# Optimization experiments

Hardware: AMD Instinct MI355X
Metric: run time of the kernel (lower is better)

The kernel has to match this reference:

```python
import jax, jax.numpy as jnp
import numpy as np

B, S, D, H = 2, 4096, 512, 8
HD = D // H


def setup_inputs() -> dict:
    key = jax.random.key(0)
    ks = jax.random.split(key, 11)
    s = 1.0 / np.sqrt(D)
    return {
        "queries": jax.random.normal(ks[0], (B, S, D), jnp.float32),
        "keys": jax.random.normal(ks[1], (B, S, D), jnp.float32),
        "values": jax.random.normal(ks[2], (B, S, D), jnp.float32),
        "Wq": jax.random.normal(ks[3], (D, D), jnp.float32) * s,
        "bq": jnp.zeros((D,), jnp.float32),
        "Wk": jax.random.normal(ks[4], (D, D), jnp.float32) * s,
        "bk": jnp.zeros((D,), jnp.float32),
        "Wv": jax.random.normal(ks[5], (D, D), jnp.float32) * s,
        "bv": jnp.zeros((D,), jnp.float32),
        "Wo": jax.random.normal(ks[6], (D, D), jnp.float32) * s,
        "bo": jnp.zeros((D,), jnp.float32),
    }


def reference(queries, keys, values, Wq, bq, Wk, bk, Wv, bv, Wo, bo):
    b = queries.shape[0]
    # Linear projections (torch Linear: x @ W.T + b; here W stored as [in, out])
    q = (queries @ Wq + bq).reshape(b, -1, H, HD)   # [B, Sq, H, HD]
    k = (keys @ Wk + bk).reshape(b, -1, H, HD)       # [B, Sk, H, HD]
    v = (values @ Wv + bv).reshape(b, -1, H, HD)     # [B, Sk, H, HD]
    logits = jnp.einsum('bqhd,bkhd->bhqk', q, k) / jnp.sqrt(jnp.float32(HD))
    attn = jax.nn.softmax(logits, axis=-1)           # [B, H, Sq, Sk]  (dropout_rate=0 -> identity)
    ctx = jnp.einsum('bhqk,bkhd->bqhd', attn, v).reshape(b, -1, H * HD)
    return ctx @ Wo + bo
```

## Files before the change

### kernel.cpp

```cpp
#include <hip/hip_runtime.h>
#include <hip/hip_bf16.h>

constexpr int B_  = 2;
constexpr int S_  = 4096;
constexpr int D_  = 512;
constexpr int H_  = 8;
constexpr int HD_ = 64;
constexpr int M_  = B_ * S_;

typedef __attribute__((ext_vector_type(8))) short short8;
typedef __attribute__((ext_vector_type(4))) float floatx4;

static __device__ __forceinline__ unsigned short f2bf(float f) {
    union { float f; unsigned u; } v; v.f = f;
    unsigned r = v.u + 0x7fffu + ((v.u >> 16) & 1u);
    return (unsigned short)(r >> 16);
}

static __device__ __forceinline__ unsigned pk2bf(float a, float b) {
#if __has_builtin(__builtin_amdgcn_cvt_pk_bf16_f32)
    typedef __attribute__((ext_vector_type(2))) __bf16 bf16x2_t;
    union { bf16x2_t v; unsigned u; } u;
    u.v = __builtin_amdgcn_cvt_pk_bf16_f32(a, b);
    return u.u;
#else
    return (unsigned)f2bf(a) | ((unsigned)f2bf(b) << 16);
#endif
}

#if __has_builtin(__builtin_amdgcn_exp2f)
#define EXP2(x) __builtin_amdgcn_exp2f(x)
#else
#define EXP2(x) exp2f(x)
#endif

#define QSCALE 0.18033688011110204f

__global__ __launch_bounds__(256) void wtrans_kernel(
    const float* __restrict__ Wq, const float* __restrict__ Wk,
    const float* __restrict__ Wv, const float* __restrict__ Wo,
    unsigned short* __restrict__ Tq, unsigned short* __restrict__ Tk,
    unsigned short* __restrict__ Tv, unsigned short* __restrict__ To) {
    const int z = blockIdx.z;
    const float* W = z == 0 ? Wq : (z == 1 ? Wk : (z == 2 ? Wv : Wo));
    unsigned short* Wt = z == 0 ? Tq : (z == 1 ? Tk : (z == 2 ? Tv : To));
    __shared__ float T[64][65];
    const int t = threadIdx.x;
    const int k0 = blockIdx.x * 64, n0 = blockIdx.y * 64;
#pragma unroll
    for (int i = 0; i < 4; ++i) {
        const int flat = t + 256 * i;
        const int kr = flat >> 4, nc = (flat & 15) * 4;
        float4 v = *(const float4*)&W[(size_t)(k0 + kr) * 512 + n0 + nc];
        T[kr][nc] = v.x; T[kr][nc + 1] = v.y; T[kr][nc + 2] = v.z; T[kr][nc + 3] = v.w;
    }
    __syncthreads();
#pragma unroll
    for (int i = 0; i < 4; ++i) {
        const int flat = t + 256 * i;
        const int nr = flat >> 4, kc = (flat & 15) * 4;
        ushort4 o4;
        o4.x = f2bf(T[kc][nr]);     o4.y = f2bf(T[kc + 1][nr]);
        o4.z = f2bf(T[kc + 2][nr]); o4.w = f2bf(T[kc + 3][nr]);
        *(ushort4*)&Wt[(size_t)(n0 + nr) * 512 + k0 + kc] = o4;
    }
}

__global__ __launch_bounds__(256, 2) void qkv_kernel(
    const float* __restrict__ Xq, const float* __restrict__ Xk, const float* __restrict__ Xv,
    const unsigned short* __restrict__ Tq, const unsigned short* __restrict__ Tk,
    const unsigned short* __restrict__ Tv,
    const float* __restrict__ bq, const float* __restrict__ bk, const float* __restrict__ bv,
    unsigned short* __restrict__ Oq, unsigned short* __restrict__ Ok,
    unsigned short* __restrict__ Ovt) {
    const int z = blockIdx.z;
    const float* A            = z == 0 ? Xq : (z == 1 ? Xk : Xv);
    const unsigned short* Wt  = z == 0 ? Tq : (z == 1 ? Tk : Tv);
    const float* bias         = z == 0 ? bq : (z == 1 ? bk : bv);
    unsigned short* out       = z == 0 ? Oq : (z == 1 ? Ok : Ovt);
    const float scale         = z == 0 ? QSCALE : 1.0f;

    const int tid = threadIdx.x;
    const int n0  = blockIdx.x * 128;
    const int m0  = blockIdx.y * 128;
    const int w   = tid >> 6;
    const int l   = tid & 63;
    const int wm  = (w >> 1) * 64;
    const int wn  = (w & 1) * 64;
    const int lm  = l & 15;
    const int lq  = l >> 4;

    const float* arow[4];
    const unsigned short* brow[4];
#pragma unroll
    for (int i = 0; i < 4; ++i) {
        arow[i] = &A[(size_t)(m0 + wm + i * 16 + lm) * 512 + lq * 8];
        brow[i] = &Wt[(size_t)(n0 + wn + i * 16 + lm) * 512 + lq * 8];
    }

    floatx4 acc[4][4];
#pragma unroll
    for (int i = 0; i < 4; ++i)
#pragma unroll
        for (int j = 0; j < 4; ++j) acc[i][j] = (floatx4)0.0f;

    float4 araw[4][2];
    short8 bnxt[4];
#pragma unroll
    for (int i = 0; i < 4; ++i) {
        araw[i][0] = *(const float4*)(arow[i]);
        araw[i][1] = *(const float4*)(arow[i] + 4);
        bnxt[i]    = *(const short8*)(brow[i]);
    }

    for (int kb = 0; kb < 16; ++kb) {
        short8 a_cur[4], b_cur[4];
#pragma unroll
        for (int i = 0; i < 4; ++i) {
            union { short8 s; unsigned u[4]; } pk;
            pk.u[0] = pk2bf(araw[i][0].x, araw[i][0].y);
            pk.u[1] = pk2bf(araw[i][0].z, araw[i][0].w);
            pk.u[2] = pk2bf(araw[i][1].x, araw[i][1].y);
            pk.u[3] = pk2bf(araw[i][1].z, araw[i][1].w);
            a_cur[i] = pk.s;
            b_cur[i] = bnxt[i];
        }
        if (kb < 15) {
            const int k1 = (kb + 1) * 32;
#pragma unroll
            for (int i = 0; i < 4; ++i) {
                araw[i][0] = *(const float4*)(arow[i] + k1);
                araw[i][1] = *(const float4*)(arow[i] + k1 + 4);
                bnxt[i]    = *(const short8*)(brow[i] + k1);
            }
        }
#pragma unroll
        for (int mi = 0; mi < 4; ++mi)
#pragma unroll
            for (int ni = 0; ni < 4; ++ni)
                acc[mi][ni] = __builtin_amdgcn_mfma_f32_16x16x32_bf16(
                    a_cur[mi], b_cur[ni], acc[mi][ni], 0, 0, 0);
    }

    float bias_n[4];
#pragma unroll
    for (int ni = 0; ni < 4; ++ni) bias_n[ni] = bias[n0 + wn + ni * 16 + lm];

#pragma unroll
    for (int mi = 0; mi < 4; ++mi) {
#pragma unroll
        for (int ni = 0; ni < 4; ++ni) {
            const int gn = n0 + wn + ni * 16 + lm;
            const int h = gn >> 6, hd = gn & 63;
            if (z == 2) {
                const int gm = m0 + wm + mi * 16 + lq * 4;
                const int b = gm >> 12, s = gm & 4095;
                ushort4 o4;
                o4.x = f2bf(acc[mi][ni][0] + bias_n[ni]);
                o4.y = f2bf(acc[mi][ni][1] + bias_n[ni]);
                o4.z = f2bf(acc[mi][ni][2] + bias_n[ni]);
                o4.w = f2bf(acc[mi][ni][3] + bias_n[ni]);
                *(ushort4*)&out[(((size_t)(b * 8 + h)) * 64 + hd) * 4096 + s] = o4;
            } else {
#pragma unroll
                for (int r = 0; r < 4; ++r) {
                    const int gm = m0 + wm + mi * 16 + lq * 4 + r;
                    const int b = gm >> 12, s = gm & 4095;
                    const float vv = (acc[mi][ni][r] + bias_n[ni]) * scale;
                    out[(((size_t)(b * 8 + h)) * 4096 + s) * 64 + hd] = f2bf(vv);
                }
            }
        }
    }
}

__global__ __launch_bounds__(512) void o_proj_kernel(
    const unsigned short* __restrict__ A, const unsigned short* __restrict__ Wt,
    const float* __restrict__ bias, float* __restrict__ outp) {
    const int tid = threadIdx.x;
    const int n0  = blockIdx.x * 128;
    const int m0  = blockIdx.y * 128;
    const int w   = tid >> 6;
    const int l   = tid & 63;
    const int wm  = (w >> 2) * 64;
    const int wn  = (w & 3) * 32;
    const int lm  = l & 15;
    const int lq  = l >> 4;

    const unsigned short* arow[4];
    const unsigned short* brow[2];
#pragma unroll
    for (int i = 0; i < 4; ++i)
        arow[i] = &A[(size_t)(m0 + wm + i * 16 + lm) * 512 + lq * 8];
#pragma unroll
    for (int i = 0; i < 2; ++i)
        brow[i] = &Wt[(size_t)(n0 + wn + i * 16 + lm) * 512 + lq * 8];

    floatx4 acc[4][2];
#pragma unroll
    for (int i = 0; i < 4; ++i)
#pragma unroll
        for (int j = 0; j < 2; ++j) acc[i][j] = (floatx4)0.0f;

    short8 anxt[4], bnxt[2];
#pragma unroll
    for (int i = 0; i < 4; ++i) anxt[i] = *(const short8*)(arow[i]);
#pragma unroll
    for (int i = 0; i < 2; ++i) bnxt[i] = *(const short8*)(brow[i]);

    for (int kb = 0; kb < 16; ++kb) {
        short8 a_cur[4], b_cur[2];
#pragma unroll
        for (int i = 0; i < 4; ++i) a_cur[i] = anxt[i];
#pragma unroll
        for (int i = 0; i < 2; ++i) b_cur[i] = bnxt[i];
        if (kb < 15) {
            const int k1 = (kb + 1) * 32;
#pragma unroll
            for (int i = 0; i < 4; ++i) anxt[i] = *(const short8*)(arow[i] + k1);
#pragma unroll
            for (int i = 0; i < 2; ++i) bnxt[i] = *(const short8*)(brow[i] + k1);
        }
#pragma unroll
        for (int mi = 0; mi < 4; ++mi)
#pragma unroll
            for (int ni = 0; ni < 2; ++ni)
                acc[mi][ni] = __builtin_amdgcn_mfma_f32_16x16x32_bf16(
                    a_cur[mi], b_cur[ni], acc[mi][ni], 0, 0, 0);
    }

    float bias_n[2];
#pragma unroll
    for (int ni = 0; ni < 2; ++ni) bias_n[ni] = bias[n0 + wn + ni * 16 + lm];

#pragma unroll
    for (int mi = 0; mi < 4; ++mi)
#pragma unroll
        for (int ni = 0; ni < 2; ++ni) {
            const int gn = n0 + wn + ni * 16 + lm;
#pragma unroll
            for (int r = 0; r < 4; ++r) {
                const int gm = m0 + wm + mi * 16 + lq * 4 + r;
                outp[(size_t)gm * 512 + gn] = acc[mi][ni][r] + bias_n[ni];
            }
        }
}

__global__ __launch_bounds__(256, 2) void flash_kernel(
    const unsigned short* __restrict__ Q, const unsigned short* __restrict__ K,
    const unsigned short* __restrict__ Vt, unsigned short* __restrict__ ctx) {
    __shared__ unsigned short Ks[64 * 64];
    __shared__ unsigned short Vs[64 * 64];
    __shared__ unsigned short Ps[4][16 * 64];

    const int tid = threadIdx.x;
    const int w   = tid >> 6;
    const int l   = tid & 63;
    const int lm  = l & 15;
    const int lq  = l >> 4;
    const int q0  = blockIdx.x * 128;
    const int bh  = blockIdx.y;

    const size_t base = (size_t)bh * S_ * HD_;
    const unsigned short* Qg = Q + base;
    const unsigned short* Kg = K + base;
    const unsigned short* Vg = Vt + base;

    short8 qf[2][2];
#pragma unroll
    for (int qn = 0; qn < 2; ++qn) {
        const unsigned short* qp = &Qg[(size_t)(q0 + w * 32 + qn * 16 + lm) * 64];
        qf[qn][0] = *(const short8*)(qp + lq * 8);
        qf[qn][1] = *(const short8*)(qp + 32 + lq * 8);
    }

    short8 ones;
#pragma unroll
    for (int j = 0; j < 8; ++j) ones[j] = (short)0x3F80;

    floatx4 o[2][4];
#pragma unroll
    for (int qn = 0; qn < 2; ++qn)
#pragma unroll
        for (int i = 0; i < 4; ++i) o[qn][i] = (floatx4)0.0f;
    floatx4 ls[2];
    ls[0] = (floatx4)0.0f; ls[1] = (floatx4)0.0f;

    const int sr  = tid >> 3, sch = tid & 7;
    const int sw0 = sr * 64 + ((sch ^ (sr & 7)) * 8);
    const int sw1 = (sr + 32) * 64 + ((sch ^ (sr & 7)) * 8);
    const int lm7 = lm & 7;

    short8 kr0, kr1, vr0, vr1;
    kr0 = *(const short8*)&Kg[(size_t)sr * 64 + sch * 8];
    kr1 = *(const short8*)&Kg[(size_t)(sr + 32) * 64 + sch * 8];
    vr0 = *(const short8*)&Vg[(size_t)sr * S_ + sch * 8];
    vr1 = *(const short8*)&Vg[(size_t)(sr + 32) * S_ + sch * 8];

    for (int kt = 0; kt < 64; ++kt) {
        __syncthreads();
        *(short8*)&Ks[sw0] = kr0;
        *(short8*)&Ks[sw1] = kr1;
        *(short8*)&Vs[sw0] = vr0;
        *(short8*)&Vs[sw1] = vr1;
        __syncthreads();
        if (kt < 63) {
            const int t1 = (kt + 1) * 64;
            kr0 = *(const short8*)&Kg[(size_t)(t1 + sr) * 64 + sch * 8];
            kr1 = *(const short8*)&Kg[(size_t)(t1 + sr + 32) * 64 + sch * 8];
            vr0 = *(const short8*)&Vg[(size_t)sr * S_ + t1 + sch * 8];
            vr1 = *(const short8*)&Vg[(size_t)(sr + 32) * S_ + t1 + sch * 8];
        }

        short8 kf[2][4];
#pragma unroll
        for (int ks = 0; ks < 2; ++ks)
#pragma unroll
            for (int ni = 0; ni < 4; ++ni)
                kf[ks][ni] = *(const short8*)&Ks[(ni * 16 + lm) * 64 +
                                                 (((ks * 4 + lq) ^ lm7) * 8)];

        floatx4 sf[2][4];
#pragma unroll
        for (int qn = 0; qn < 2; ++qn)
#pragma unroll
            for (int ni = 0; ni < 4; ++ni) sf[qn][ni] = (floatx4)0.0f;
#pragma unroll
        for (int ks = 0; ks < 2; ++ks)
#pragma unroll
            for (int qn = 0; qn < 2; ++qn)
#pragma unroll
                for (int ni = 0; ni < 4; ++ni)
                    sf[qn][ni] = __builtin_amdgcn_mfma_f32_16x16x32_bf16(
                        kf[ks][ni], qf[qn][ks], sf[qn][ni], 0, 0, 0);

        short8 vf[2][4];
#pragma unroll
        for (int c = 0; c < 2; ++c)
#pragma unroll
            for (int ni = 0; ni < 4; ++ni)
                vf[c][ni] = *(const short8*)&Vs[(ni * 16 + lm) * 64 +
                                                (((c * 4 + lq) ^ lm7) * 8)];

        unsigned short* Pw = &Ps[w][0];
#pragma unroll
        for (int qn = 0; qn < 2; ++qn) {
#pragma unroll
            for (int ni = 0; ni < 4; ++ni) {
                uint2 pv;
                pv.x = pk2bf(EXP2(sf[qn][ni][0]), EXP2(sf[qn][ni][1]));
                pv.y = pk2bf(EXP2(sf[qn][ni][2]), EXP2(sf[qn][ni][3]));
                *(uint2*)&Pw[lm * 64 + (((ni * 2 + (lq >> 1)) ^ lm7) * 8) + (lq & 1) * 4] = pv;
            }
#pragma unroll
            for (int c = 0; c < 2; ++c) {
                short8 pf = *(const short8*)&Pw[lm * 64 + (((c * 4 + lq) ^ lm7) * 8)];
                ls[qn] = __builtin_amdgcn_mfma_f32_16x16x32_bf16(ones, pf, ls[qn], 0, 0, 0);
#pragma unroll
                for (int ni = 0; ni < 4; ++ni)
                    o[qn][ni] = __builtin_amdgcn_mfma_f32_16x16x32_bf16(
                        vf[c][ni], pf, o[qn][ni], 0, 0, 0);
            }
        }
    }

    const int b = bh >> 3, h = bh & 7;
#pragma unroll
    for (int qn = 0; qn < 2; ++qn) {
        const float inv = 1.0f / ls[qn][0];
        const int q = q0 + w * 32 + qn * 16 + lm;
        const size_t rb = ((size_t)(b * S_ + q)) * 512 + h * 64;
#pragma unroll
        for (int ni = 0; ni < 4; ++ni) {
            union { ushort4 s; uint2 u; } o4;
            o4.u.x = pk2bf(o[qn][ni][0] * inv, o[qn][ni][1] * inv);
            o4.u.y = pk2bf(o[qn][ni][2] * inv, o[qn][ni][3] * inv);
            *(ushort4*)&ctx[rb + ni * 16 + lq * 4] = o4.s;
        }
    }
}

extern "C" void kernel_launch(void* const* d_in, const int* in_sizes, int n_in,
                              void* d_out, int out_size, void* d_ws, size_t ws_size,
                              hipStream_t stream) {
    const float* queries = (const float*)d_in[0];
    const float* keys    = (const float*)d_in[1];
    const float* values  = (const float*)d_in[2];
    const float* Wq = (const float*)d_in[3];
    const float* bq = (const float*)d_in[4];
    const float* Wk = (const float*)d_in[5];
    const float* bk = (const float*)d_in[6];
    const float* Wv = (const float*)d_in[7];
    const float* bv = (const float*)d_in[8];
    const float* Wo = (const float*)d_in[9];
    const float* bo = (const float*)d_in[10];

    unsigned short* wsq   = (unsigned short*)d_ws;
    unsigned short* wsk   = wsq   + (size_t)M_ * D_;
    unsigned short* wsvt  = wsk   + (size_t)M_ * D_;
    unsigned short* wsctx = wsvt  + (size_t)M_ * D_;
    unsigned short* wtq   = wsctx + (size_t)M_ * D_;
    unsigned short* wtk   = wtq   + (size_t)D_ * D_;
    unsigned short* wtv   = wtk   + (size_t)D_ * D_;
    unsigned short* wto   = wtv   + (size_t)D_ * D_;

    wtrans_kernel<<<dim3(8, 8, 4), dim3(256), 0, stream>>>(
        Wq, Wk, Wv, Wo, wtq, wtk, wtv, wto);

    qkv_kernel<<<dim3(D_ / 128, M_ / 128, 3), dim3(256), 0, stream>>>(
        queries, keys, values, wtq, wtk, wtv, bq, bk, bv, wsq, wsk, wsvt);

    flash_kernel<<<dim3(S_ / 128, B_ * H_), dim3(256), 0, stream>>>(wsq, wsk, wsvt, wsctx);

    o_proj_kernel<<<dim3(D_ / 128, M_ / 128), dim3(512), 0, stream>>>(
        wsctx, wto, bo, (float*)d_out);
}
```

Measured before the change: 291.3 us.

## Pre-cast inputs to bf16 and use LDS-staged swizzled GEMM for projections

Adds a separate kernel that casts the fp32 query/key/value inputs to bf16 once. The QKV and output projections now share one templated GEMM that stages 128x64 A and B tiles into shared memory with direct global-to-LDS loads and an XOR swizzle. Before, each wave read its operands straight from global memory and converted fp32 to bf16 inside the loop. Tiles are now shared across waves in a block, in exchange for an extra pass over the inputs and two syncthreads per k-step with no double buffering. Because the weight transposes are laid out contiguously, the QKV GEMM indexes Wq, Wk and Wv through a single pointer.

```diff
diff --git a/kernel.cpp b/kernel.cpp
--- a/kernel.cpp
+++ b/kernel.cpp
@@ -35,6 +35,31 @@
 #endif
 
 #define QSCALE 0.18033688011110204f
+
+static __device__ __forceinline__ void gl_lds16(const void* g, void* l) {
+    typedef __attribute__((address_space(1))) const unsigned GU;
+    typedef __attribute__((address_space(3))) unsigned LU;
+    __builtin_amdgcn_global_load_lds((GU*)g, (LU*)l, 16, 0, 0);
+}
+
+__global__ __launch_bounds__(256) void xcast_kernel(
+    const float* __restrict__ Xq, const float* __restrict__ Xk, const float* __restrict__ Xv,
+    unsigned short* __restrict__ Y) {
+    const int z = blockIdx.z;
+    const float* X = z == 0 ? Xq : (z == 1 ? Xk : Xv);
+    unsigned short* Yz = Y + (size_t)z * M_ * D_;
+    const int n8 = M_ * D_ / 8;
+    int i = blockIdx.x * 256 + threadIdx.x;
+    const int stride = gridDim.x * 256;
+    for (; i < n8; i += stride) {
+        float4 a = *(const float4*)&X[(size_t)i * 8];
+        float4 b = *(const float4*)&X[(size_t)i * 8 + 4];
+        union { short8 s; unsigned u[4]; } p;
+        p.u[0] = pk2bf(a.x, a.y); p.u[1] = pk2bf(a.z, a.w);
+        p.u[2] = pk2bf(b.x, b.y); p.u[3] = pk2bf(b.z, b.w);
+        *(short8*)&Yz[(size_t)i * 8] = p.s;
+    }
+}
 
 __global__ __launch_bounds__(256) void wtrans_kernel(
     const float* __restrict__ Wq, const float* __restrict__ Wk,
@@ -66,37 +91,32 @@
     }
 }
 
-__global__ __launch_bounds__(256, 2) void qkv_kernel(
-    const float* __restrict__ Xq, const float* __restrict__ Xk, const float* __restrict__ Xv,
-    const unsigned short* __restrict__ Tq, const unsigned short* __restrict__ Tk,
-    const unsigned short* __restrict__ Tv,
-    const float* __restrict__ bq, const float* __restrict__ bk, const float* __restrict__ bv,
-    unsigned short* __restrict__ Oq, unsigned short* __restrict__ Ok,
-    unsigned short* __restrict__ Ovt) {
-    const int z = blockIdx.z;
-    const float* A            = z == 0 ? Xq : (z == 1 ? Xk : Xv);
-    const unsigned short* Wt  = z == 0 ? Tq : (z == 1 ? Tk : Tv);
-    const float* bias         = z == 0 ? bq : (z == 1 ? bk : bv);
-    unsigned short* out       = z == 0 ? Oq : (z == 1 ? Ok : Ovt);
-    const float scale         = z == 0 ? QSCALE : 1.0f;
-
-    const int tid = threadIdx.x;
-    const int n0  = blockIdx.x * 128;
-    const int m0  = blockIdx.y * 128;
-    const int w   = tid >> 6;
-    const int l   = tid & 63;
-    const int wm  = (w >> 1) * 64;
-    const int wn  = (w & 1) * 64;
-    const int lm  = l & 15;
-    const int lq  = l >> 4;
-
-    const float* arow[4];
-    const unsigned short* brow[4];
-#pragma unroll
-    for (int i = 0; i < 4; ++i) {
-        arow[i] = &A[(size_t)(m0 + wm + i * 16 + lm) * 512 + lq * 8];
-        brow[i] = &Wt[(size_t)(n0 + wn + i * 16 + lm) * 512 + lq * 8];
-    }
+template <int MODE>
+__global__ __launch_bounds__(256, 3) void gemm_kernel(
+    const unsigned short* __restrict__ Ab,
+    const unsigned short* __restrict__ Wt,
+    const float* __restrict__ b0, const float* __restrict__ b1, const float* __restrict__ b2,
+    unsigned short* __restrict__ o0, unsigned short* __restrict__ o1,
+    unsigned short* __restrict__ o2, float* __restrict__ of) {
+    __shared__ unsigned short As[128 * 64];
+    __shared__ unsigned short Bs[128 * 64];
+
+    const int tid  = threadIdx.x;
+    const int w    = tid >> 6;
+    const int lane = tid & 63;
+    const int n0   = blockIdx.x * 128;
+    const int m0   = blockIdx.y * 128;
+    const int lm   = lane & 15;
+    const int lq   = lane >> 4;
+    const int wm   = (w >> 1) * 64;
+    const int wn   = (w & 1) * 64;
+
+    const int z = MODE == 0 ? (n0 >> 9) : 0;
+    const unsigned short* A = MODE == 0 ? Ab + (size_t)z * M_ * D_ : Ab;
+
+    const int srow = lane >> 3;
+    const int sch  = lane & 7;
+    const int ca   = (sch ^ (srow & 7)) * 8;
 
     floatx4 acc[4][4];
 #pragma unroll
@@ -104,146 +124,78 @@
 #pragma unroll
         for (int j = 0; j < 4; ++j) acc[i][j] = (floatx4)0.0f;
 
-    float4 araw[4][2];
-    short8 bnxt[4];
-#pragma unroll
-    for (int i = 0; i < 4; ++i) {
-        araw[i][0] = *(const float4*)(arow[i]);
-        araw[i][1] = *(const float4*)(arow[i] + 4);
-        bnxt[i]    = *(const short8*)(brow[i]);
-    }
-
-    for (int kb = 0; kb < 16; ++kb) {
-        short8 a_cur[4], b_cur[4];
-#pragma unroll
-        for (int i = 0; i < 4; ++i) {
-            union { short8 s; unsigned u[4]; } pk;
-            pk.u[0] = pk2bf(araw[i][0].x, araw[i][0].y);
-            pk.u[1] = pk2bf(araw[i][0].z, araw[i][0].w);
-            pk.u[2] = pk2bf(araw[i][1].x, araw[i][1].y);
-            pk.u[3] = pk2bf(araw[i][1].z, araw[i][1].w);
-            a_cur[i] = pk.s;
-            b_cur[i] = bnxt[i];
-        }
-        if (kb < 15) {
-            const int k1 = (kb + 1) * 32;
+    for (int kb = 0; kb < 8; ++kb) {
+        const int k0 = kb * 64;
+        __syncthreads();
+#pragma unroll
+        for (int it = 0; it < 4; ++it) {
+            const int r8 = w * 32 + it * 8;
+            gl_lds16(&A [(size_t)(m0 + r8 + srow) * 512 + k0 + ca], &As[r8 * 64]);
+            gl_lds16(&Wt[(size_t)(n0 + r8 + srow) * 512 + k0 + ca], &Bs[r8 * 64]);
+        }
+        __syncthreads();
+
+        short8 af[2][4], bf[2][4];
+#pragma unroll
+        for (int ks = 0; ks < 2; ++ks)
 #pragma unroll
             for (int i = 0; i < 4; ++i) {
-                araw[i][0] = *(const float4*)(arow[i] + k1);
-                araw[i][1] = *(const float4*)(arow[i] + k1 + 4);
-                bnxt[i]    = *(const short8*)(brow[i] + k1);
+                const int cc = ((ks * 4 + lq) ^ (lm & 7)) * 8;
+                af[ks][i] = *(const short8*)&As[(wm + i * 16 + lm) * 64 + cc];
+                bf[ks][i] = *(const short8*)&Bs[(wn + i * 16 + lm) * 64 + cc];
             }
-        }
-#pragma unroll
-        for (int mi = 0; mi < 4; ++mi)
-#pragma unroll
-            for (int ni = 0; ni < 4; ++ni)
-                acc[mi][ni] = __builtin_amdgcn_mfma_f32_16x16x32_bf16(
-                    a_cur[mi], b_cur[ni], acc[mi][ni], 0, 0, 0);
-    }
+#pragma unroll
+        for (int ks = 0; ks < 2; ++ks)
+#pragma unroll
+            for (int mi = 0; mi < 4; ++mi)
+#pragma unroll
+                for (int ni = 0; ni < 4; ++ni)
+                    acc[mi][ni] = __builtin_amdgcn_mfma_f32_16x16x32_bf16(
+                        af[ks][mi], bf[ks][ni], acc[mi][ni], 0, 0, 0);
+    }
+
+    const float* bias = MODE == 0 ? (z == 0 ? b0 : (z == 1 ? b1 : b2)) : b0;
+    const float scale = (MODE == 0 && z == 0) ? QSCALE : 1.0f;
+    const int nl0 = n0 & 511;
 
     float bias_n[4];
 #pragma unroll
-    for (int ni = 0; ni < 4; ++ni) bias_n[ni] = bias[n0 + wn + ni * 16 + lm];
+    for (int ni = 0; ni < 4; ++ni) bias_n[ni] = bias[nl0 + wn + ni * 16 + lm];
 
 #pragma unroll
     for (int mi = 0; mi < 4; ++mi) {
 #pragma unroll
         for (int ni = 0; ni < 4; ++ni) {
-            const int gn = n0 + wn + ni * 16 + lm;
-            const int h = gn >> 6, hd = gn & 63;
-            if (z == 2) {
-                const int gm = m0 + wm + mi * 16 + lq * 4;
-                const int b = gm >> 12, s = gm & 4095;
-                ushort4 o4;
-                o4.x = f2bf(acc[mi][ni][0] + bias_n[ni]);
-                o4.y = f2bf(acc[mi][ni][1] + bias_n[ni]);
-                o4.z = f2bf(acc[mi][ni][2] + bias_n[ni]);
-                o4.w = f2bf(acc[mi][ni][3] + bias_n[ni]);
-                *(ushort4*)&out[(((size_t)(b * 8 + h)) * 64 + hd) * 4096 + s] = o4;
-            } else {
+            if (MODE == 1) {
+                const int gn = n0 + wn + ni * 16 + lm;
 #pragma unroll
                 for (int r = 0; r < 4; ++r) {
                     const int gm = m0 + wm + mi * 16 + lq * 4 + r;
+                    of[(size_t)gm * 512 + gn] = acc[mi][ni][r] + bias_n[ni];
+                }
+            } else {
+                const int gnl = nl0 + wn + ni * 16 + lm;
+                const int h = gnl >> 6, hd = gnl & 63;
+                if (z == 2) {
+                    const int gm = m0 + wm + mi * 16 + lq * 4;
                     const int b = gm >> 12, s = gm & 4095;
-                    const float vv = (acc[mi][ni][r] + bias_n[ni]) * scale;
-                    out[(((size_t)(b * 8 + h)) * 4096 + s) * 64 + hd] = f2bf(vv);
+                    union { ushort4 s4; uint2 u; } o4;
+                    o4.u.x = pk2bf(acc[mi][ni][0] + bias_n[ni], acc[mi][ni][1] + bias_n[ni]);
+                    o4.u.y = pk2bf(acc[mi][ni][2] + bias_n[ni], acc[mi][ni][3] + bias_n[ni]);
+                    *(ushort4*)&o2[(((size_t)(b * 8 + h)) * 64 + hd) * 4096 + s] = o4.s4;
+                } else {
+                    unsigned short* out = z == 0 ? o0 : o1;
+#pragma unroll
+                    for (int r = 0; r < 4; ++r) {
+                        const int gm = m0 + wm + mi * 16 + lq * 4 + r;
+                        const int b = gm >> 12, s = gm & 4095;
+                        const float vv = (acc[mi][ni][r] + bias_n[ni]) * scale;
+                        out[(((size_t)(b * 8 + h)) * 4096 + s) * 64 + hd] = f2bf(vv);
+                    }
                 }
             }
         }
     }
-}
-
-__global__ __launch_bounds__(512) void o_proj_kernel(
-    const unsigned short* __restrict__ A, const unsigned short* __restrict__ Wt,
-    const float* __restrict__ bias, float* __restrict__ outp) {
-    const int tid = threadIdx.x;
-    const int n0  = blockIdx.x * 128;
-    const int m0  = blockIdx.y * 128;
-    const int w   = tid >> 6;
-    const int l   = tid & 63;
-    const int wm  = (w >> 2) * 64;
-    const int wn  = (w & 3) * 32;
-    const int lm  = l & 15;
-    const int lq  = l >> 4;
-
-    const unsigned short* arow[4];
-    const unsigned short* brow[2];
-#pragma unroll
-    for (int i = 0; i < 4; ++i)
-        arow[i] = &A[(size_t)(m0 + wm + i * 16 + lm) * 512 + lq * 8];
-#pragma unroll
-    for (int i = 0; i < 2; ++i)
-        brow[i] = &Wt[(size_t)(n0 + wn + i * 16 + lm) * 512 + lq * 8];
-
-    floatx4 acc[4][2];
-#pragma unroll
-    for (int i = 0; i < 4; ++i)
-#pragma unroll
-        for (int j = 0; j < 2; ++j) acc[i][j] = (floatx4)0.0f;
-
-    short8 anxt[4], bnxt[2];
-#pragma unroll
-    for (int i = 0; i < 4; ++i) anxt[i] = *(const short8*)(arow[i]);
-#pragma unroll
-    for (int i = 0; i < 2; ++i) bnxt[i] = *(const short8*)(brow[i]);
-
-    for (int kb = 0; kb < 16; ++kb) {
-        short8 a_cur[4], b_cur[2];
-#pragma unroll
-        for (int i = 0; i < 4; ++i) a_cur[i] = anxt[i];
-#pragma unroll
-        for (int i = 0; i < 2; ++i) b_cur[i] = bnxt[i];
-        if (kb < 15) {
-            const int k1 = (kb + 1) * 32;
-#pragma unroll
-            for (int i = 0; i < 4; ++i) anxt[i] = *(const short8*)(arow[i] + k1);
-#pragma unroll
-            for (int i = 0; i < 2; ++i) bnxt[i] = *(const short8*)(brow[i] + k1);
-        }
-#pragma unroll
-        for (int mi = 0; mi < 4; ++mi)
-#pragma unroll
-            for (int ni = 0; ni < 2; ++ni)
-                acc[mi][ni] = __builtin_amdgcn_mfma_f32_16x16x32_bf16(
-                    a_cur[mi], b_cur[ni], acc[mi][ni], 0, 0, 0);
-    }
-
-    float bias_n[2];
-#pragma unroll
-    for (int ni = 0; ni < 2; ++ni) bias_n[ni] = bias[n0 + wn + ni * 16 + lm];
-
-#pragma unroll
-    for (int mi = 0; mi < 4; ++mi)
-#pragma unroll
-        for (int ni = 0; ni < 2; ++ni) {
-            const int gn = n0 + wn + ni * 16 + lm;
-#pragma unroll
-            for (int r = 0; r < 4; ++r) {
-                const int gm = m0 + wm + mi * 16 + lq * 4 + r;
-                outp[(size_t)gm * 512 + gn] = acc[mi][ni][r] + bias_n[ni];
-            }
-        }
 }
 
 __global__ __launch_bounds__(256, 2) void flash_kernel(
@@ -395,23 +347,25 @@
     const float* Wo = (const float*)d_in[9];
     const float* bo = (const float*)d_in[10];
 
-    unsigned short* wsq   = (unsigned short*)d_ws;
-    unsigned short* wsk   = wsq   + (size_t)M_ * D_;
-    unsigned short* wsvt  = wsk   + (size_t)M_ * D_;
-    unsigned short* wsctx = wsvt  + (size_t)M_ * D_;
-    unsigned short* wtq   = wsctx + (size_t)M_ * D_;
-    unsigned short* wtk   = wtq   + (size_t)D_ * D_;
-    unsigned short* wtv   = wtk   + (size_t)D_ * D_;
-    unsigned short* wto   = wtv   + (size_t)D_ * D_;
-
+    unsigned short* xb    = (unsigned short*)d_ws;
+    unsigned short* wsctx = xb;
+    unsigned short* wsq   = xb   + (size_t)3 * M_ * D_;
+    unsigned short* wsk   = wsq  + (size_t)M_ * D_;
+    unsigned short* wsvt  = wsk  + (size_t)M_ * D_;
+    unsigned short* wtq   = wsvt + (size_t)M_ * D_;
+    unsigned short* wtk   = wtq  + (size_t)D_ * D_;
+    unsigned short* wtv   = wtk  + (size_t)D_ * D_;
+    unsigned short* wto   = wtv  + (size_t)D_ * D_;
+
+    xcast_kernel<<<dim3(1024, 1, 3), dim3(256), 0, stream>>>(queries, keys, values, xb);
     wtrans_kernel<<<dim3(8, 8, 4), dim3(256), 0, stream>>>(
         Wq, Wk, Wv, Wo, wtq, wtk, wtv, wto);
 
-    qkv_kernel<<<dim3(D_ / 128, M_ / 128, 3), dim3(256), 0, stream>>>(
-        queries, keys, values, wtq, wtk, wtv, bq, bk, bv, wsq, wsk, wsvt);
+    gemm_kernel<0><<<dim3(12, 64), dim3(256), 0, stream>>>(
+        xb, wtq, bq, bk, bv, wsq, wsk, wsvt, nullptr);
 
     flash_kernel<<<dim3(S_ / 128, B_ * H_), dim3(256), 0, stream>>>(wsq, wsk, wsvt, wsctx);
 
-    o_proj_kernel<<<dim3(D_ / 128, M_ / 128), dim3(512), 0, stream>>>(
-        wsctx, wto, bo, (float*)d_out);
-}
+    gemm_kernel<1><<<dim3(4, 64), dim3(256), 0, stream>>>(
+        wsctx, wto, bo, nullptr, nullptr, nullptr, nullptr, nullptr, (float*)d_out);
+}
```

Measured after the change: 243.8 us. 16.3% less time.
